# Kernel optimization log

Hardware: AMD Instinct MI355X
Metric: run time of the kernel (lower is better)

Reference implementation:

```python
import jax, jax.numpy as jnp
import numpy as np

N_NODES = 50000
N_EDGES = 800000
D_IN = 128
D_HID = 128
D_OUT = 128
N_GRAPHS = 64


def _gcn_conv(x, src, dst, W, b, n_nodes):
    """PyG GCNConv: D^{-1/2} (A + I) D^{-1/2} X W + b (self-loops added)."""
    xw = x @ W  # [N, F_out]
    loops = jnp.arange(n_nodes, dtype=src.dtype)
    s = jnp.concatenate([src, loops])  # sources (messages gathered here)
    d = jnp.concatenate([dst, loops])  # targets (aggregation index)
    ones = jnp.ones_like(d, dtype=xw.dtype)
    deg = jax.ops.segment_sum(ones, d, num_segments=n_nodes)  # in-degree incl. self-loop
    dinv = jnp.where(deg > 0, jax.lax.rsqrt(deg), 0.0)
    norm = dinv[s] * dinv[d]  # [E+N]
    msg = xw[s] * norm[:, None]  # gather + scale
    out = jax.ops.segment_sum(msg, d, num_segments=n_nodes)  # scatter-add
    return out + b


def _global_mean_pool(x, batch, num_graphs):
    sums = jax.ops.segment_sum(x, batch, num_segments=num_graphs)
    cnts = jax.ops.segment_sum(jnp.ones((x.shape[0],), x.dtype), batch, num_segments=num_graphs)
    return sums / jnp.maximum(cnts, 1.0)[:, None]


def setup_inputs() -> dict:
    key = jax.random.key(0)
    k = jax.random.split(key, 8)
    x = jax.random.normal(k[0], (N_NODES, D_IN), dtype=jnp.float32)
    edge_index = jax.random.randint(k[1], (2, N_EDGES), 0, N_NODES, dtype=jnp.int64)
    batch = jnp.sort(jax.random.randint(k[2], (N_NODES,), 0, N_GRAPHS, dtype=jnp.int64))
    # Glorot-ish params for the two GCNConv layers
    W1 = jax.random.normal(k[3], (D_IN, D_HID), dtype=jnp.float32) / np.sqrt(D_IN)
    b1 = jnp.zeros((D_HID,), dtype=jnp.float32)
    W2 = jax.random.normal(k[4], (D_HID, D_OUT), dtype=jnp.float32) / np.sqrt(D_HID)
    b2 = jnp.zeros((D_OUT,), dtype=jnp.float32)
    return {"x": x, "edge_index": edge_index, "batch": batch,
            "W1": W1, "b1": b1, "W2": W2, "b2": b2}


def reference(x, edge_index, batch, W1, b1, W2, b2):
    src, dst = edge_index[0], edge_index[1]
    n = x.shape[0]
    h = _gcn_conv(x, src, dst, W1, b1, n)
    h = jax.nn.relu(h)
    h = _gcn_conv(h, src, dst, W2, b2, n)
    return _global_mean_pool(h, batch, N_GRAPHS)  # [N_GRAPHS, D_OUT]
```

## Files before the change

kernel.cpp:

```cpp
#include <hip/hip_runtime.h>
#include <hip/hip_bf16.h>

#define SPAN_SHIFT 8
#define BCAP 8192

typedef __attribute__((ext_vector_type(8))) short short8;
typedef __attribute__((ext_vector_type(4))) float float4v;

__device__ __forceinline__ float bf2f(unsigned short u) {
  union { unsigned int i; float f; } v; v.i = ((unsigned int)u) << 16; return v.f;
}
__device__ __forceinline__ unsigned short f2bf(float f) {
  union { float f; unsigned int i; } v; v.f = f;
  unsigned int x = v.i;
  return (unsigned short)((x + 0x7fffu + ((x >> 16) & 1u)) >> 16);
}

__global__ __launch_bounds__(256) void detect_zero_k(
    const unsigned short* __restrict__ xu,  const int* __restrict__ ei,
    const unsigned short* __restrict__ w1u, const unsigned short* __restrict__ w2u,
    const unsigned short* __restrict__ b1u, const unsigned short* __restrict__ b2u,
    int* __restrict__ flags, int* __restrict__ bcnt, float* __restrict__ acc,
    int NB, int GP) {
  const int b = blockIdx.x;
  if (b >= 6) {
    int base = (b - 6) * 4096 + threadIdx.x;
    #pragma unroll
    for (int j = 0; j < 16; ++j) {
      int i = base + j * 256;
      if (i < NB) bcnt[i] = 0;
      else if (i < NB + GP) acc[i - NB] = 0.f;
    }
    return;
  }
  __shared__ int s_cnt;
  if (threadIdx.x == 0) s_cnt = 0;
  __syncthreads();
  int cnt = 0;
  if (b == 1) {
    for (int i = threadIdx.x; i < 4096; i += 256)
      if (ei[2 * i + 1] == 0) cnt++;
    atomicAdd(&s_cnt, cnt);
    __syncthreads();
    if (threadIdx.x == 0) flags[1] = (s_cnt > 2048) ? 1 : 0;
    return;
  }
  const unsigned short* p; int n; int fi;
  if (b == 0)      { p = xu;  n = 16384; fi = 0; }
  else if (b == 2) { p = w1u; n = 16384; fi = 2; }
  else if (b == 3) { p = w2u; n = 16384; fi = 3; }
  else if (b == 4) { p = b1u; n = 128;   fi = 4; }
  else             { p = b2u; n = 128;   fi = 5; }
  for (int i = threadIdx.x; i < n; i += 256) {
    int e = (p[i] >> 7) & 0xFF;
    if (e < 96 || e > 159) cnt++;
  }
  atomicAdd(&s_cnt, cnt);
  __syncthreads();
  if (threadIdx.x == 0) flags[fi] = (s_cnt * 8 > n) ? 1 : 0;
}

__global__ __launch_bounds__(256) void swizzle_w_k(const void* __restrict__ W1,
    const void* __restrict__ W2, unsigned short* __restrict__ w1s,
    unsigned short* __restrict__ w2s, const int* __restrict__ flags) {
  const int b = blockIdx.x;
  const void* Wraw = (b < 64) ? W1 : W2;
  unsigned short* out = (b < 64) ? w1s : w2s;
  const int wf32 = (b < 64) ? flags[2] : flags[3];
  int u = (b & 63) * 256 + threadIdx.x;
  int j = u & 7, lane = (u >> 3) & 63, blk = u >> 9;
  int c = blk >> 3, t = blk & 7;
  int quad = lane >> 4, col = lane & 15;
  int k = c * 32 + quad * 8 + j;
  int n = t * 16 + col;
  out[u] = wf32 ? f2bf(((const float*)Wraw)[k * 128 + n])
                : ((const unsigned short*)Wraw)[k * 128 + n];
}

__global__ __launch_bounds__(256) void gemm_k(const void* __restrict__ X,
                                              const unsigned short* __restrict__ Wsw,
                                              unsigned short* __restrict__ XWb, int N,
                                              const int* __restrict__ flags, int xmode) {
  __shared__ __align__(16) unsigned short Wl[16384];
  __shared__ __align__(16) unsigned short Xl[64 * 136];
  const int tid = threadIdx.x;
  const int xf32 = xmode ? 1 : flags[0];
  const int row0 = blockIdx.x * 64;
  for (int v = tid; v < 2048; v += 256)
    ((short8*)Wl)[v] = ((const short8*)Wsw)[v];
  for (int v = tid; v < 2048; v += 256) {
    int r = v >> 5, k4 = (v & 31) * 4;
    int row = row0 + r;
    ushort4 u = make_ushort4(0, 0, 0, 0);
    if (row < N) {
      long long gi = (long long)row * 128 + k4;
      if (xf32) {
        float4 xv = *(const float4*)&((const float*)X)[gi];
        u.x = f2bf(xv.x); u.y = f2bf(xv.y); u.z = f2bf(xv.z); u.w = f2bf(xv.w);
      } else {
        u = *(const ushort4*)&((const unsigned short*)X)[gi];
      }
    }
    *(ushort4*)&Xl[r * 136 + k4] = u;
  }
  __syncthreads();
  const int w = tid >> 6, lane = tid & 63;
  const int quad = lane >> 4, col = lane & 15;
  float4v acc[8];
  #pragma unroll
  for (int t = 0; t < 8; ++t) acc[t] = (float4v){0.f, 0.f, 0.f, 0.f};
  #pragma unroll
  for (int c = 0; c < 4; ++c) {
    short8 a = *(const short8*)&Xl[(w * 16 + col) * 136 + c * 32 + quad * 8];
    #pragma unroll
    for (int t = 0; t < 8; ++t) {
      short8 b = *(const short8*)&Wl[((c * 8 + t) * 64 + lane) * 8];
      acc[t] = __builtin_amdgcn_mfma_f32_16x16x32_bf16(a, b, acc[t], 0, 0, 0);
    }
  }
  #pragma unroll
  for (int t = 0; t < 8; ++t) {
    #pragma unroll
    for (int r = 0; r < 4; ++r)
      Xl[(w * 16 + quad * 4 + r) * 136 + t * 16 + col] = f2bf(acc[t][r]);
  }
  __syncthreads();
  for (int v = tid; v < 1024; v += 256) {
    int r = v >> 4, ck = (v & 15) * 8;
    int row = row0 + r;
    if (row < N)
      *(short8*)&XWb[(long long)row * 128 + ck] = *(const short8*)&Xl[r * 136 + ck];
  }
}

__global__ __launch_bounds__(256) void scatterA_k(const int* __restrict__ ei,
    int* __restrict__ bcnt, int2* __restrict__ tmp, int E,
    const int* __restrict__ flags, int NBKT) {
  __shared__ int2 stage[4096];
  __shared__ int hist[256], off[256], cnt2[256], gbase[256];
  __shared__ int wsum[4];
  const int tid = threadIdx.x;
  hist[tid] = 0; cnt2[tid] = 0;
  __syncthreads();
  const int base = blockIdx.x * 4096;
  const int i64 = flags[1];
  int rs[16], rd[16];
  #pragma unroll
  for (int j = 0; j < 16; ++j) {
    int e = base + j * 256 + tid;
    if (e < E) {
      int s, d;
      if (i64) { s = ei[2 * e]; d = ei[2 * (E + e)]; }
      else     { s = ei[e];     d = ei[E + e]; }
      rs[j] = s; rd[j] = d;
      atomicAdd(&hist[d >> SPAN_SHIFT], 1);
    } else rd[j] = -1;
  }
  __syncthreads();
  {
    int lane = tid & 63, w = tid >> 6;
    int v = hist[tid], inc = v;
    #pragma unroll
    for (int o = 1; o < 64; o <<= 1) { int n = __shfl_up(inc, o, 64); if (lane >= o) inc += n; }
    if (lane == 63) wsum[w] = inc;
    __syncthreads();
    int pre = 0;
    #pragma unroll
    for (int k = 0; k < 4; ++k) if (k < w) pre += wsum[k];
    off[tid] = pre + inc - v;
  }
  __syncthreads();
  #pragma unroll
  for (int j = 0; j < 16; ++j) {
    if (rd[j] >= 0) {
      int b = rd[j] >> SPAN_SHIFT;
      int r = atomicAdd(&cnt2[b], 1);
      int2 rec; rec.x = rs[j]; rec.y = rd[j];
      stage[off[b] + r] = rec;
    }
  }
  if (tid < NBKT && hist[tid] > 0)
    gbase[tid] = tid * BCAP + atomicAdd(&bcnt[tid], hist[tid]);
  __syncthreads();
  const int total = off[255] + hist[255];
  for (int i = tid; i < total; i += 256) {
    int2 rec = stage[i];
    int b = rec.y >> SPAN_SHIFT;
    tmp[gbase[b] + (i - off[b])] = rec;
  }
}

__global__ __launch_bounds__(256) void bucket_scan_k(const int* __restrict__ bcnt,
    int* __restrict__ bbase, int* __restrict__ rowptrN, int NBKT, int E) {
  __shared__ int ws[4];
  const int tid = threadIdx.x, lane = tid & 63, w = tid >> 6;
  int v = (tid < NBKT) ? bcnt[tid] : 0;
  int inc = v;
  #pragma unroll
  for (int off = 1; off < 64; off <<= 1) {
    int n = __shfl_up(inc, off, 64);
    if (lane >= off) inc += n;
  }
  if (lane == 63) ws[w] = inc;
  __syncthreads();
  int pre = 0;
  #pragma unroll
  for (int k = 0; k < 4; ++k) if (k < w) pre += ws[k];
  if (tid < NBKT) bbase[tid] = pre + inc - v;
  if (tid == 0) *rowptrN = E;
}

__global__ __launch_bounds__(256) void scatB1_k(const int2* __restrict__ tmp,
    const int* __restrict__ bcnt, const int* __restrict__ bbase,
    int* __restrict__ rowptr, float* __restrict__ dinv, int N) {
  __shared__ int hist[256];
  __shared__ int ws[4];
  const int tid = threadIdx.x;
  const int b = blockIdx.x;
  hist[tid] = 0;
  __syncthreads();
  const int cnt = bcnt[b];
  const int2* src = tmp + (long long)b * BCAP;
  for (int i = tid; i < cnt; i += 256)
    atomicAdd(&hist[src[i].y & 255], 1);
  __syncthreads();
  int v = hist[tid], inc = v;
  int lane = tid & 63, w = tid >> 6;
  #pragma unroll
  for (int off = 1; off < 64; off <<= 1) {
    int n = __shfl_up(inc, off, 64);
    if (lane >= off) inc += n;
  }
  if (lane == 63) ws[w] = inc;
  __syncthreads();
  int pre = 0;
  #pragma unroll
  for (int k = 0; k < 4; ++k) if (k < w) pre += ws[k];
  int node = (b << SPAN_SHIFT) + tid;
  if (node < N) {
    rowptr[node] = bbase[b] + pre + inc - v;
    dinv[node] = rsqrtf((float)(v + 1));
  }
}

__global__ __launch_bounds__(256) void scatB2_k(const int2* __restrict__ tmp,
    const int* __restrict__ bcnt, const int* __restrict__ rowptr,
    const float* __restrict__ dinv, int2* __restrict__ spk, int N) {
  __shared__ int cur[256];
  const int tid = threadIdx.x;
  const int b = blockIdx.x;
  const int n0 = b << SPAN_SHIFT;
  if (n0 + tid < N) cur[tid] = rowptr[n0 + tid];
  __syncthreads();
  const int cnt = bcnt[b];
  const int2* src = tmp + (long long)b * BCAP;
  for (int i = tid; i < cnt; i += 256) {
    int2 rec = src[i];
    int pos = atomicAdd(&cur[rec.y & 255], 1);
    int2 out; out.x = rec.x; out.y = __float_as_int(dinv[rec.x]);
    spk[pos] = out;
  }
}

__global__ __launch_bounds__(256) void aggregate_k(const unsigned short* __restrict__ XWb,
    const int* __restrict__ rowptr, const int2* __restrict__ spk,
    const float* __restrict__ dinv, const void* __restrict__ bias_raw, int bias_fi,
    float* __restrict__ H, int N, int relu, const int* __restrict__ flags) {
  int wid = (blockIdx.x * 256 + threadIdx.x) >> 6;
  if (wid >= N) return;
  const int lane = threadIdx.x & 63;
  const int half = lane >> 5;
  const int fl = (lane & 31) * 4;
  const int beg = rowptr[wid], end = rowptr[wid + 1];
  const float di = dinv[wid];
  float a0 = 0.f, a1 = 0.f, a2 = 0.f, a3 = 0.f;
  int idx = beg;
  for (; idx + 8 <= end; idx += 8) {
    int2 rA = spk[idx + half];
    int2 rB = spk[idx + 2 + half];
    int2 rC = spk[idx + 4 + half];
    int2 rD = spk[idx + 6 + half];
    float wA = __int_as_float(rA.y), wB = __int_as_float(rB.y);
    float wC = __int_as_float(rC.y), wD = __int_as_float(rD.y);
    ushort4 uA = *(const ushort4*)&XWb[(long long)rA.x * 128 + fl];
    ushort4 uB = *(const ushort4*)&XWb[(long long)rB.x * 128 + fl];
    ushort4 uC = *(const ushort4*)&XWb[(long long)rC.x * 128 + fl];
    ushort4 uD = *(const ushort4*)&XWb[(long long)rD.x * 128 + fl];
    a0 += wA * bf2f(uA.x) + wB * bf2f(uB.x) + wC * bf2f(uC.x) + wD * bf2f(uD.x);
    a1 += wA * bf2f(uA.y) + wB * bf2f(uB.y) + wC * bf2f(uC.y) + wD * bf2f(uD.y);
    a2 += wA * bf2f(uA.z) + wB * bf2f(uB.z) + wC * bf2f(uC.z) + wD * bf2f(uD.z);
    a3 += wA * bf2f(uA.w) + wB * bf2f(uB.w) + wC * bf2f(uC.w) + wD * bf2f(uD.w);
  }
  if (idx + 4 <= end) {
    int2 rA = spk[idx + half];
    int2 rB = spk[idx + 2 + half];
    float wA = __int_as_float(rA.y), wB = __int_as_float(rB.y);
    ushort4 uA = *(const ushort4*)&XWb[(long long)rA.x * 128 + fl];
    ushort4 uB = *(const ushort4*)&XWb[(long long)rB.x * 128 + fl];
    a0 += wA * bf2f(uA.x) + wB * bf2f(uB.x);
    a1 += wA * bf2f(uA.y) + wB * bf2f(uB.y);
    a2 += wA * bf2f(uA.z) + wB * bf2f(uB.z);
    a3 += wA * bf2f(uA.w) + wB * bf2f(uB.w);
    idx += 4;
  }
  if (idx < end) {
    int iA = idx + half;
    int2 rA = spk[min(iA, end - 1)];
    float wA = (iA < end) ? __int_as_float(rA.y) : 0.f;
    ushort4 uA = *(const ushort4*)&XWb[(long long)rA.x * 128 + fl];
    a0 += wA * bf2f(uA.x); a1 += wA * bf2f(uA.y);
    a2 += wA * bf2f(uA.z); a3 += wA * bf2f(uA.w);
    if (idx + 2 < end) {
      int iB = idx + 2 + half;
      int2 rB = spk[min(iB, end - 1)];
      float wB = (iB < end) ? __int_as_float(rB.y) : 0.f;
      ushort4 uB = *(const ushort4*)&XWb[(long long)rB.x * 128 + fl];
      a0 += wB * bf2f(uB.x); a1 += wB * bf2f(uB.y);
      a2 += wB * bf2f(uB.z); a3 += wB * bf2f(uB.w);
    }
  }
  a0 += __shfl_xor(a0, 32, 64);
  a1 += __shfl_xor(a1, 32, 64);
  a2 += __shfl_xor(a2, 32, 64);
  a3 += __shfl_xor(a3, 32, 64);
  if (half == 0) {
    ushort4 su = *(const ushort4*)&XWb[(long long)wid * 128 + fl];
    float d2 = di * di;
    float o0 = di * a0 + d2 * bf2f(su.x);
    float o1 = di * a1 + d2 * bf2f(su.y);
    float o2 = di * a2 + d2 * bf2f(su.z);
    float o3 = di * a3 + d2 * bf2f(su.w);
    if (bias_fi >= 0) {
      if (flags[bias_fi]) {
        float4 bv = *(const float4*)&((const float*)bias_raw)[fl];
        o0 += bv.x; o1 += bv.y; o2 += bv.z; o3 += bv.w;
      } else {
        const unsigned short* bu = (const unsigned short*)bias_raw;
        o0 += bf2f(bu[fl]); o1 += bf2f(bu[fl + 1]);
        o2 += bf2f(bu[fl + 2]); o3 += bf2f(bu[fl + 3]);
      }
    }
    if (relu) {
      o0 = fmaxf(o0, 0.f); o1 = fmaxf(o1, 0.f);
      o2 = fmaxf(o2, 0.f); o3 = fmaxf(o3, 0.f);
    }
    *(float4*)&H[(long long)wid * 128 + fl] = make_float4(o0, o1, o2, o3);
  }
}

__global__ __launch_bounds__(256) void pool_partial_k(const float* __restrict__ H,
    const int* __restrict__ batch, float* __restrict__ acc, int N,
    const int* __restrict__ flags) {
  const int i64 = flags[1];
  const int lane = threadIdx.x & 63;
  const int w = threadIdx.x >> 6;
  const int chunk = (N + gridDim.x - 1) / gridDim.x;
  const int bstart = blockIdx.x * chunk;
  const int bend = min(bstart + chunk, N);
  const int sub = (chunk + 3) / 4;
  const int s = bstart + w * sub;
  const int e = min(s + sub, bend);
  if (s >= e) return;
  float ax = 0.f, ay = 0.f;
  int curg = i64 ? batch[2 * s] : batch[s];
  for (int n = s; n < e; ++n) {
    int g = i64 ? batch[2 * n] : batch[n];
    if (g != curg) {
      atomicAdd(&acc[curg * 128 + lane * 2], ax);
      atomicAdd(&acc[curg * 128 + lane * 2 + 1], ay);
      ax = ay = 0.f; curg = g;
    }
    float2 v = *(const float2*)&H[(long long)n * 128 + lane * 2];
    ax += v.x; ay += v.y;
  }
  atomicAdd(&acc[curg * 128 + lane * 2], ax);
  atomicAdd(&acc[curg * 128 + lane * 2 + 1], ay);
}

__global__ __launch_bounds__(128) void pool_final_k(const float* __restrict__ acc,
    const int* __restrict__ batch, const void* __restrict__ B2raw,
    float* __restrict__ out, int N, const int* __restrict__ flags) {
  __shared__ int sb[2];
  int g = blockIdx.x;
  int i64 = flags[1];
  if (threadIdx.x < 2) {
    int target = g + threadIdx.x;
    int lo = 0, hi = N;
    while (lo < hi) {
      int mid = (lo + hi) >> 1;
      int bv = i64 ? batch[2 * mid] : batch[mid];
      if (bv < target) lo = mid + 1; else hi = mid;
    }
    sb[threadIdx.x] = lo;
  }
  __syncthreads();
  int cnt = sb[1] - sb[0];
  int f = threadIdx.x;
  float b2 = flags[5] ? ((const float*)B2raw)[f]
                      : bf2f(((const unsigned short*)B2raw)[f]);
  float res = 0.f;
  if (cnt > 0) res = acc[g * 128 + f] / (float)cnt + b2;
  out[g * 128 + f] = res;
}

extern "C" void kernel_launch(void* const* d_in, const int* in_sizes, int n_in,
                              void* d_out, int out_size, void* d_ws, size_t ws_size,
                              hipStream_t stream) {
  const int N = in_sizes[0] / 128;
  const int E = in_sizes[1] / 2;
  const int G = out_size / 128;
  const int NB = (N + 255) >> SPAN_SHIFT;
  const int GB = (N + 63) / 64;
  const int ZB = (NB + G * 128 + 4095) / 4096;

  const void* X  = d_in[0];
  const int*  EI = (const int*)d_in[1];
  const int*  BA = (const int*)d_in[2];
  const void* W1 = d_in[3];
  const void* B1 = d_in[4];
  const void* W2 = d_in[5];
  const void* B2 = d_in[6];
  float* OUT = (float*)d_out;

  char* ws = (char*)d_ws;
  size_t o = 0;
  auto alloc = [&](size_t b) { size_t r = o; o += (b + 255) & ~(size_t)255; return r; };
  int*   flags  = (int*)(ws + alloc(256));
  unsigned short* w1s = (unsigned short*)(ws + alloc(16384 * 2));
  unsigned short* w2s = (unsigned short*)(ws + alloc(16384 * 2));
  float* acc    = (float*)(ws + alloc((size_t)G * 128 * 4));
  int*   bcnt   = (int*)(ws + alloc(256 * 4));
  int*   bbase  = (int*)(ws + alloc(256 * 4));
  int*   rowptr = (int*)(ws + alloc((size_t)(N + 1) * 4));
  int2*  spk    = (int2*)(ws + alloc((size_t)E * 8));
  float* dinv   = (float*)(ws + alloc((size_t)N * 4));
  unsigned short* xwb = (unsigned short*)(ws + alloc((size_t)N * 128 * 2));
  float* h1     = (float*)(ws + alloc((size_t)N * 128 * 4));
  float* h2     = h1;
  int2*  tmp    = (int2*)h1;

  detect_zero_k<<<6 + ZB, 256, 0, stream>>>((const unsigned short*)X, EI,
                                            (const unsigned short*)W1, (const unsigned short*)W2,
                                            (const unsigned short*)B1, (const unsigned short*)B2,
                                            flags, bcnt, acc, NB, G * 128);
  swizzle_w_k<<<128, 256, 0, stream>>>(W1, W2, w1s, w2s, flags);
  gemm_k<<<GB, 256, 0, stream>>>(X, w1s, xwb, N, flags, 0);
  scatterA_k<<<(E + 4095) / 4096, 256, 0, stream>>>(EI, bcnt, tmp, E, flags, NB);
  bucket_scan_k<<<1, 256, 0, stream>>>(bcnt, bbase, rowptr + N, NB, E);
  scatB1_k<<<NB, 256, 0, stream>>>(tmp, bcnt, bbase, rowptr, dinv, N);
  scatB2_k<<<NB, 256, 0, stream>>>(tmp, bcnt, rowptr, dinv, spk, N);

  dim3 agrid((N * 64 + 255) / 256);
  aggregate_k<<<agrid, 256, 0, stream>>>(xwb, rowptr, spk, dinv, B1, 4, h1, N, 1, flags);
  gemm_k<<<GB, 256, 0, stream>>>(h1, w2s, xwb, N, flags, 1);
  aggregate_k<<<agrid, 256, 0, stream>>>(xwb, rowptr, spk, dinv, (const void*)nullptr, -1,
                                         h2, N, 0, flags);
  pool_partial_k<<<512, 256, 0, stream>>>(h2, BA, acc, N, flags);
  pool_final_k<<<G, 128, 0, stream>>>(acc, BA, B2, OUT, N, flags);
}
```

Before: 245.9 us.

## Merge small setup kernels and co-schedule edge bucketing with first GEMM

The weight swizzle now runs inside the detection/zeroing kernel, with each block checking its own weight dtype. The edge bucket scatter and the first GEMM share one launch using a block-index split. The single-block bucket scan is folded into scatB1, where each block recomputes the prefix. The first layer's hidden activations are written as bf16 instead of fp32, which halves that write and the second GEMM's read. Together this removes three launches and some memory traffic, at the cost of redundant scans and a larger shared-memory footprint for the fused kernel.

```diff
diff --git a/kernel.cpp b/kernel.cpp
--- a/kernel.cpp
+++ b/kernel.cpp
@@ -16,76 +16,78 @@
   return (unsigned short)((x + 0x7fffu + ((x >> 16) & 1u)) >> 16);
 }
 
-__global__ __launch_bounds__(256) void detect_zero_k(
+__global__ __launch_bounds__(256) void detect_swz_zero_k(
     const unsigned short* __restrict__ xu,  const int* __restrict__ ei,
-    const unsigned short* __restrict__ w1u, const unsigned short* __restrict__ w2u,
     const unsigned short* __restrict__ b1u, const unsigned short* __restrict__ b2u,
+    const void* __restrict__ W1, const void* __restrict__ W2,
+    unsigned short* __restrict__ w1s, unsigned short* __restrict__ w2s,
     int* __restrict__ flags, int* __restrict__ bcnt, float* __restrict__ acc,
-    int NB, int GP) {
+    int NBKT, int GP) {
   const int b = blockIdx.x;
-  if (b >= 6) {
-    int base = (b - 6) * 4096 + threadIdx.x;
+  const int tid = threadIdx.x;
+  if (b >= 132) {
+    int base = (b - 132) * 4096 + tid;
     #pragma unroll
     for (int j = 0; j < 16; ++j) {
       int i = base + j * 256;
-      if (i < NB) bcnt[i] = 0;
-      else if (i < NB + GP) acc[i - NB] = 0.f;
+      if (i < NBKT) bcnt[i] = 0;
+      else if (i < NBKT + GP) acc[i - NBKT] = 0.f;
     }
     return;
   }
   __shared__ int s_cnt;
-  if (threadIdx.x == 0) s_cnt = 0;
-  __syncthreads();
+  if (tid == 0) s_cnt = 0;
+  __syncthreads();
+  if (b >= 4) {
+    const void* Wraw = (b < 68) ? W1 : W2;
+    unsigned short* out = (b < 68) ? w1s : w2s;
+    const unsigned short* Wu = (const unsigned short*)Wraw;
+    int c = 0;
+    for (int i = tid; i < 512; i += 256) {
+      int e = (Wu[i] >> 7) & 0xFF;
+      if (e < 96 || e > 159) c++;
+    }
+    atomicAdd(&s_cnt, c);
+    __syncthreads();
+    const int wf32 = s_cnt > 64;
+    int u = ((b - 4) & 63) * 256 + tid;
+    int j = u & 7, lane = (u >> 3) & 63, blk = u >> 9;
+    int cc = blk >> 3, t = blk & 7;
+    int quad = lane >> 4, col = lane & 15;
+    int k = cc * 32 + quad * 8 + j;
+    int n = t * 16 + col;
+    out[u] = wf32 ? f2bf(((const float*)Wraw)[k * 128 + n])
+                  : ((const unsigned short*)Wraw)[k * 128 + n];
+    return;
+  }
   int cnt = 0;
   if (b == 1) {
-    for (int i = threadIdx.x; i < 4096; i += 256)
+    for (int i = tid; i < 4096; i += 256)
       if (ei[2 * i + 1] == 0) cnt++;
     atomicAdd(&s_cnt, cnt);
     __syncthreads();
-    if (threadIdx.x == 0) flags[1] = (s_cnt > 2048) ? 1 : 0;
+    if (tid == 0) flags[1] = (s_cnt > 2048) ? 1 : 0;
     return;
   }
   const unsigned short* p; int n; int fi;
   if (b == 0)      { p = xu;  n = 16384; fi = 0; }
-  else if (b == 2) { p = w1u; n = 16384; fi = 2; }
-  else if (b == 3) { p = w2u; n = 16384; fi = 3; }
-  else if (b == 4) { p = b1u; n = 128;   fi = 4; }
+  else if (b == 2) { p = b1u; n = 128;   fi = 4; }
   else             { p = b2u; n = 128;   fi = 5; }
-  for (int i = threadIdx.x; i < n; i += 256) {
+  for (int i = tid; i < n; i += 256) {
     int e = (p[i] >> 7) & 0xFF;
     if (e < 96 || e > 159) cnt++;
   }
   atomicAdd(&s_cnt, cnt);
   __syncthreads();
-  if (threadIdx.x == 0) flags[fi] = (s_cnt * 8 > n) ? 1 : 0;
-}
-
-__global__ __launch_bounds__(256) void swizzle_w_k(const void* __restrict__ W1,
-    const void* __restrict__ W2, unsigned short* __restrict__ w1s,
-    unsigned short* __restrict__ w2s, const int* __restrict__ flags) {
-  const int b = blockIdx.x;
-  const void* Wraw = (b < 64) ? W1 : W2;
-  unsigned short* out = (b < 64) ? w1s : w2s;
-  const int wf32 = (b < 64) ? flags[2] : flags[3];
-  int u = (b & 63) * 256 + threadIdx.x;
-  int j = u & 7, lane = (u >> 3) & 63, blk = u >> 9;
-  int c = blk >> 3, t = blk & 7;
-  int quad = lane >> 4, col = lane & 15;
-  int k = c * 32 + quad * 8 + j;
-  int n = t * 16 + col;
-  out[u] = wf32 ? f2bf(((const float*)Wraw)[k * 128 + n])
-                : ((const unsigned short*)Wraw)[k * 128 + n];
-}
-
-__global__ __launch_bounds__(256) void gemm_k(const void* __restrict__ X,
-                                              const unsigned short* __restrict__ Wsw,
-                                              unsigned short* __restrict__ XWb, int N,
-                                              const int* __restrict__ flags, int xmode) {
-  __shared__ __align__(16) unsigned short Wl[16384];
-  __shared__ __align__(16) unsigned short Xl[64 * 136];
+  if (tid == 0) flags[fi] = (s_cnt * 8 > n) ? 1 : 0;
+}
+
+__device__ __forceinline__ void gemm_body(const void* __restrict__ X,
+                                          const unsigned short* __restrict__ Wsw,
+                                          unsigned short* __restrict__ XWb, int N,
+                                          int xf32, int row0,
+                                          unsigned short* Wl, unsigned short* Xl) {
   const int tid = threadIdx.x;
-  const int xf32 = xmode ? 1 : flags[0];
-  const int row0 = blockIdx.x * 64;
   for (int v = tid; v < 2048; v += 256)
     ((short8*)Wl)[v] = ((const short8*)Wsw)[v];
   for (int v = tid; v < 2048; v += 256) {
@@ -133,13 +135,25 @@
   }
 }
 
-__global__ __launch_bounds__(256) void scatterA_k(const int* __restrict__ ei,
-    int* __restrict__ bcnt, int2* __restrict__ tmp, int E,
+__global__ __launch_bounds__(256) void scatA_gemm1_k(const int* __restrict__ ei,
+    int* __restrict__ bcnt, int2* __restrict__ tmp, int E, int SA,
+    const void* __restrict__ X, const unsigned short* __restrict__ Wsw,
+    unsigned short* __restrict__ XWb, int N,
     const int* __restrict__ flags, int NBKT) {
-  __shared__ int2 stage[4096];
-  __shared__ int hist[256], off[256], cnt2[256], gbase[256];
-  __shared__ int wsum[4];
+  __shared__ __align__(16) char smem[50688];
   const int tid = threadIdx.x;
+  if ((int)blockIdx.x >= SA) {
+    unsigned short* Wl = (unsigned short*)smem;
+    unsigned short* Xl = (unsigned short*)(smem + 32768);
+    gemm_body(X, Wsw, XWb, N, flags[0], ((int)blockIdx.x - SA) * 64, Wl, Xl);
+    return;
+  }
+  int2* stage = (int2*)smem;
+  int* hist  = (int*)(smem + 32768);
+  int* off   = hist + 256;
+  int* cnt2  = off + 256;
+  int* gbase = cnt2 + 256;
+  int* wsum  = gbase + 256;
   hist[tid] = 0; cnt2[tid] = 0;
   __syncthreads();
   const int base = blockIdx.x * 4096;
@@ -190,46 +204,49 @@
   }
 }
 
-__global__ __launch_bounds__(256) void bucket_scan_k(const int* __restrict__ bcnt,
-    int* __restrict__ bbase, int* __restrict__ rowptrN, int NBKT, int E) {
-  __shared__ int ws[4];
-  const int tid = threadIdx.x, lane = tid & 63, w = tid >> 6;
-  int v = (tid < NBKT) ? bcnt[tid] : 0;
-  int inc = v;
-  #pragma unroll
-  for (int off = 1; off < 64; off <<= 1) {
-    int n = __shfl_up(inc, off, 64);
-    if (lane >= off) inc += n;
-  }
-  if (lane == 63) ws[w] = inc;
-  __syncthreads();
-  int pre = 0;
-  #pragma unroll
-  for (int k = 0; k < 4; ++k) if (k < w) pre += ws[k];
-  if (tid < NBKT) bbase[tid] = pre + inc - v;
-  if (tid == 0) *rowptrN = E;
+__global__ __launch_bounds__(256) void gemm_k(const void* __restrict__ X,
+                                              const unsigned short* __restrict__ Wsw,
+                                              unsigned short* __restrict__ XWb, int N,
+                                              int xmode) {
+  __shared__ __align__(16) unsigned short Wl[16384];
+  __shared__ __align__(16) unsigned short Xl[64 * 136];
+  gemm_body(X, Wsw, XWb, N, (xmode == 1) ? 1 : 0, blockIdx.x * 64, Wl, Xl);
 }
 
 __global__ __launch_bounds__(256) void scatB1_k(const int2* __restrict__ tmp,
-    const int* __restrict__ bcnt, const int* __restrict__ bbase,
-    int* __restrict__ rowptr, float* __restrict__ dinv, int N) {
+    const int* __restrict__ bcnt, int* __restrict__ rowptr,
+    float* __restrict__ dinv, int N, int NBKT, int E) {
   __shared__ int hist[256];
+  __shared__ int pfx[256];
   __shared__ int ws[4];
   const int tid = threadIdx.x;
   const int b = blockIdx.x;
+  const int lane = tid & 63, w = tid >> 6;
+  int c = (tid < NBKT) ? bcnt[tid] : 0;
   hist[tid] = 0;
-  __syncthreads();
+  {
+    int inc = c;
+    #pragma unroll
+    for (int o = 1; o < 64; o <<= 1) { int n = __shfl_up(inc, o, 64); if (lane >= o) inc += n; }
+    if (lane == 63) ws[w] = inc;
+    __syncthreads();
+    int pre = 0;
+    #pragma unroll
+    for (int k = 0; k < 4; ++k) if (k < w) pre += ws[k];
+    pfx[tid] = pre + inc - c;
+  }
+  __syncthreads();
+  const int bbase = pfx[b];
   const int cnt = bcnt[b];
   const int2* src = tmp + (long long)b * BCAP;
   for (int i = tid; i < cnt; i += 256)
     atomicAdd(&hist[src[i].y & 255], 1);
   __syncthreads();
   int v = hist[tid], inc = v;
-  int lane = tid & 63, w = tid >> 6;
-  #pragma unroll
-  for (int off = 1; off < 64; off <<= 1) {
-    int n = __shfl_up(inc, off, 64);
-    if (lane >= off) inc += n;
+  #pragma unroll
+  for (int o = 1; o < 64; o <<= 1) {
+    int n = __shfl_up(inc, o, 64);
+    if (lane >= o) inc += n;
   }
   if (lane == 63) ws[w] = inc;
   __syncthreads();
@@ -238,9 +255,10 @@
   for (int k = 0; k < 4; ++k) if (k < w) pre += ws[k];
   int node = (b << SPAN_SHIFT) + tid;
   if (node < N) {
-    rowptr[node] = bbase[b] + pre + inc - v;
+    rowptr[node] = bbase + pre + inc - v;
     dinv[node] = rsqrtf((float)(v + 1));
   }
+  if (b == 0 && tid == 0) rowptr[N] = E;
 }
 
 __global__ __launch_bounds__(256) void scatB2_k(const int2* __restrict__ tmp,
@@ -265,7 +283,8 @@
 __global__ __launch_bounds__(256) void aggregate_k(const unsigned short* __restrict__ XWb,
     const int* __restrict__ rowptr, const int2* __restrict__ spk,
     const float* __restrict__ dinv, const void* __restrict__ bias_raw, int bias_fi,
-    float* __restrict__ H, int N, int relu, const int* __restrict__ flags) {
+    void* __restrict__ H, int N, int relu, int out_bf16,
+    const int* __restrict__ flags) {
   int wid = (blockIdx.x * 256 + threadIdx.x) >> 6;
   if (wid >= N) return;
   const int lane = threadIdx.x & 63;
@@ -344,7 +363,13 @@
       o0 = fmaxf(o0, 0.f); o1 = fmaxf(o1, 0.f);
       o2 = fmaxf(o2, 0.f); o3 = fmaxf(o3, 0.f);
     }
-    *(float4*)&H[(long long)wid * 128 + fl] = make_float4(o0, o1, o2, o3);
+    if (out_bf16) {
+      ushort4 uo;
+      uo.x = f2bf(o0); uo.y = f2bf(o1); uo.z = f2bf(o2); uo.w = f2bf(o3);
+      *(ushort4*)&((unsigned short*)H)[(long long)wid * 128 + fl] = uo;
+    } else {
+      *(float4*)&((float*)H)[(long long)wid * 128 + fl] = make_float4(o0, o1, o2, o3);
+    }
   }
 }
 
@@ -411,6 +436,7 @@
   const int G = out_size / 128;
   const int NB = (N + 255) >> SPAN_SHIFT;
   const int GB = (N + 63) / 64;
+  const int SA = (E + 4095) / 4096;
   const int ZB = (NB + G * 128 + 4095) / 4096;
 
   const void* X  = d_in[0];
@@ -430,31 +456,30 @@
   unsigned short* w2s = (unsigned short*)(ws + alloc(16384 * 2));
   float* acc    = (float*)(ws + alloc((size_t)G * 128 * 4));
   int*   bcnt   = (int*)(ws + alloc(256 * 4));
-  int*   bbase  = (int*)(ws + alloc(256 * 4));
   int*   rowptr = (int*)(ws + alloc((size_t)(N + 1) * 4));
   int2*  spk    = (int2*)(ws + alloc((size_t)E * 8));
   float* dinv   = (float*)(ws + alloc((size_t)N * 4));
   unsigned short* xwb = (unsigned short*)(ws + alloc((size_t)N * 128 * 2));
-  float* h1     = (float*)(ws + alloc((size_t)N * 128 * 4));
-  float* h2     = h1;
-  int2*  tmp    = (int2*)h1;
-
-  detect_zero_k<<<6 + ZB, 256, 0, stream>>>((const unsigned short*)X, EI,
-                                            (const unsigned short*)W1, (const unsigned short*)W2,
-                                            (const unsigned short*)B1, (const unsigned short*)B2,
-                                            flags, bcnt, acc, NB, G * 128);
-  swizzle_w_k<<<128, 256, 0, stream>>>(W1, W2, w1s, w2s, flags);
-  gemm_k<<<GB, 256, 0, stream>>>(X, w1s, xwb, N, flags, 0);
-  scatterA_k<<<(E + 4095) / 4096, 256, 0, stream>>>(EI, bcnt, tmp, E, flags, NB);
-  bucket_scan_k<<<1, 256, 0, stream>>>(bcnt, bbase, rowptr + N, NB, E);
-  scatB1_k<<<NB, 256, 0, stream>>>(tmp, bcnt, bbase, rowptr, dinv, N);
+  char*  hreg   = ws + alloc((size_t)N * 128 * 4);
+  unsigned short* h1b = (unsigned short*)hreg;
+  float* h2f    = (float*)hreg;
+  int2*  tmp    = (int2*)hreg;
+
+  detect_swz_zero_k<<<132 + ZB, 256, 0, stream>>>(
+      (const unsigned short*)X, EI,
+      (const unsigned short*)B1, (const unsigned short*)B2,
+      W1, W2, w1s, w2s, flags, bcnt, acc, NB, G * 128);
+  scatA_gemm1_k<<<SA + GB, 256, 0, stream>>>(EI, bcnt, tmp, E, SA,
+                                             X, w1s, xwb, N, flags, NB);
+  scatB1_k<<<NB, 256, 0, stream>>>(tmp, bcnt, rowptr, dinv, N, NB, E);
   scatB2_k<<<NB, 256, 0, stream>>>(tmp, bcnt, rowptr, dinv, spk, N);
 
   dim3 agrid((N * 64 + 255) / 256);
-  aggregate_k<<<agrid, 256, 0, stream>>>(xwb, rowptr, spk, dinv, B1, 4, h1, N, 1, flags);
-  gemm_k<<<GB, 256, 0, stream>>>(h1, w2s, xwb, N, flags, 1);
+  aggregate_k<<<agrid, 256, 0, stream>>>(xwb, rowptr, spk, dinv, B1, 4,
+                                         h1b, N, 1, 1, flags);
+  gemm_k<<<GB, 256, 0, stream>>>(h1b, w2s, xwb, N, 2);
   aggregate_k<<<agrid, 256, 0, stream>>>(xwb, rowptr, spk, dinv, (const void*)nullptr, -1,
-                                         h2, N, 0, flags);
-  pool_partial_k<<<512, 256, 0, stream>>>(h2, BA, acc, N, flags);
+                                         h2f, N, 0, 0, flags);
+  pool_partial_k<<<512, 256, 0, stream>>>(h2f, BA, acc, N, flags);
   pool_final_k<<<G, 128, 0, stream>>>(acc, BA, B2, OUT, N, flags);
 }
```

Result: faster. 229.9 us (-6.5%).
